# Performance work log

Hardware: AMD Instinct MI355X
Metric: run time of the kernel (lower is better)

Reference implementation:

```python
import jax, jax.numpy as jnp
import numpy as np

N, K, H, E_IN = 4096, 48, 128, 384
SCALE = 30.0
EPS = 1e-5


def _gelu(x):
    return jax.nn.gelu(x, approximate=False)


def _ln(x, s, o):
    m = jnp.mean(x, axis=-1, keepdims=True)
    v = jnp.var(x, axis=-1, keepdims=True)
    return (x - m) * jax.lax.rsqrt(v + EPS) * s + o


def setup_inputs() -> dict:
    key = jax.random.key(0)
    ks = jax.random.split(key, 12)
    init = lambda k, shp: (jax.random.normal(k, shp, jnp.float32) * 0.02)
    return {
        "h_V": jax.random.normal(ks[0], (N, H), jnp.float32),
        "h_E": jax.random.normal(ks[1], (N, K, E_IN), jnp.float32),
        "mask_V": jnp.ones((N,), jnp.float32),
        "mask_attend": jnp.ones((N, K), jnp.float32),
        "W1_w": init(ks[2], (H + E_IN, H)), "W1_b": jnp.zeros((H,), jnp.float32),
        "W2_w": init(ks[3], (H, H)), "W2_b": jnp.zeros((H,), jnp.float32),
        "W3_w": init(ks[4], (H, H)), "W3_b": jnp.zeros((H,), jnp.float32),
        "Win_w": init(ks[5], (H, 4 * H)), "Win_b": jnp.zeros((4 * H,), jnp.float32),
        "Wout_w": init(ks[6], (4 * H, H)), "Wout_b": jnp.zeros((H,), jnp.float32),
        "norm1_s": jnp.ones((H,), jnp.float32), "norm1_o": jnp.zeros((H,), jnp.float32),
        "norm2_s": jnp.ones((H,), jnp.float32), "norm2_o": jnp.zeros((H,), jnp.float32),
    }


def reference(h_V, h_E, mask_V, mask_attend,
              W1_w, W1_b, W2_w, W2_b, W3_w, W3_b,
              Win_w, Win_b, Wout_w, Wout_b,
              norm1_s, norm1_o, norm2_s, norm2_o):
    # expand node features over K neighbors and concat with edge features: [N,K,H+E_IN]
    h_V_expand = jnp.broadcast_to(h_V[:, None, :], (h_V.shape[0], h_E.shape[1], h_V.shape[1]))
    h_EV = jnp.concatenate([h_V_expand, h_E], axis=-1)
    # 3-layer GELU MLP on each edge token
    h = _gelu(jnp.einsum('nke,eh->nkh', h_EV, W1_w) + W1_b)
    h = _gelu(jnp.einsum('nkh,hg->nkg', h, W2_w) + W2_b)
    h_message = jnp.einsum('nkg,gh->nkh', h, W3_w) + W3_b
    # masked sum-reduce over neighbors
    h_message = mask_attend[..., None] * h_message
    dh = jnp.sum(h_message, axis=-2) / SCALE
    h_Vn = _ln(h_V + dh, norm1_s, norm1_o)  # dropout rate = 0.0 -> identity
    # position-wise FFN
    dh = _gelu(h_Vn @ Win_w + Win_b) @ Wout_w + Wout_b
    h_Vn = _ln(h_Vn + dh, norm2_s, norm2_o)
    return mask_V[:, None] * h_Vn
```

## Files before the change

kernel.cpp:

```cpp
#include <hip/hip_runtime.h>
#include <hip/hip_bf16.h>
#include <math.h>

typedef __attribute__((ext_vector_type(8))) __bf16 bf16x8;
typedef __attribute__((ext_vector_type(4))) float f32x4;

#define OFF_W1P    0
#define OFF_W2P    65536
#define OFF_W3P    81920
#define OFF_WINP   98304
#define OFF_WOUTP  163840
#define NPACK      229376
#define OFF_DH_BYTES 458752

__device__ __forceinline__ float gelu_f(float x) {
  float t = 1.5957691216f * x * (1.0f + 0.044715f * x * x);
  return __fdividef(x, 1.0f + __expf(-t));
}

__device__ __forceinline__ bf16x8 cvt8(float4 u, float4 v) {
  bf16x8 r;
  r[0] = (__bf16)u.x; r[1] = (__bf16)u.y; r[2] = (__bf16)u.z; r[3] = (__bf16)u.w;
  r[4] = (__bf16)v.x; r[5] = (__bf16)v.y; r[6] = (__bf16)v.z; r[7] = (__bf16)v.w;
  return r;
}

__device__ __forceinline__ void gload_lds16(const void* g, void* l) {
  __builtin_amdgcn_global_load_lds(
      (const __attribute__((address_space(1))) void*)g,
      (__attribute__((address_space(3))) void*)l, 16, 0, 0);
}

#define MFMA __builtin_amdgcn_mfma_f32_16x16x32_bf16

__global__ __launch_bounds__(256) void prep_kernel(
    const float* __restrict__ W1, const float* __restrict__ W2,
    const float* __restrict__ W3, const float* __restrict__ Wi,
    const float* __restrict__ Wo, __bf16* __restrict__ wsb)
{
  int i = blockIdx.x * 256 + threadIdx.x;
  float v;
  if (i < 65536) {
    int j = i;
    int jj = j & 7, ln = (j >> 3) & 63, n = (j >> 9) & 7, ks = j >> 12;
    int k = ks * 32 + (ln >> 4) * 8 + jj, h = n * 16 + (ln & 15);
    v = W1[k * 128 + h];
  } else if (i < 81920) {
    int j = i - 65536;
    int jj = j & 7, ln = (j >> 3) & 63, n = (j >> 9) & 7, ks = j >> 12;
    int k = ks * 32 + (ln >> 4) * 8 + jj, g = n * 16 + (ln & 15);
    v = W2[k * 128 + g];
  } else if (i < 98304) {
    int j = i - 81920;
    int jj = j & 7, ln = (j >> 3) & 63, n = (j >> 9) & 7, ks = j >> 12;
    int k = ks * 32 + (ln >> 4) * 8 + jj, h = n * 16 + (ln & 15);
    v = W3[k * 128 + h];
  } else if (i < 163840) {
    int j = i - 98304;
    int jj = j & 7, ln = (j >> 3) & 63, n = (j >> 9) & 31, ks = j >> 14;
    int k = ks * 32 + (ln >> 4) * 8 + jj, o = n * 16 + (ln & 15);
    v = Wi[k * 512 + o];
  } else {
    int j = i - 163840;
    int jj = j & 7, ln = (j >> 3) & 63, n = (j >> 9) & 7, ks = j >> 12;
    int k = ks * 32 + (ln >> 4) * 8 + jj, h = n * 16 + (ln & 15);
    v = Wo[k * 128 + h];
  }
  wsb[i] = (__bf16)v;
}

__global__ __launch_bounds__(256, 4) void edge_mlp_kernel(
    const float* __restrict__ hE, const float* __restrict__ hV,
    const float* __restrict__ mask_att, const __bf16* __restrict__ wsb,
    const float* __restrict__ b1, const float* __restrict__ b2,
    const float* __restrict__ b3, float* __restrict__ dh)
{
  __shared__ char lds[24576];

  const int tid = threadIdx.x;
  const int w = tid >> 6, lane = tid & 63;
  const int lo = lane & 15, hi = lane >> 4;
  const int n0 = blockIdx.x * 2;

  const __bf16* W1p = wsb + OFF_W1P;

  f32x4 acc[2][3][2];
#pragma unroll
  for (int nl = 0; nl < 2; nl++)
#pragma unroll
    for (int m = 0; m < 3; m++)
#pragma unroll
      for (int nn = 0; nn < 2; nn++) {
        acc[nl][m][nn][0] = 0.f; acc[nl][m][nn][1] = 0.f;
        acc[nl][m][nn][2] = 0.f; acc[nl][m][nn][3] = 0.f;
      }

  const char* gsrc[3];
  int ldst[3];
#pragma unroll
  for (int j = 0; j < 3; j++) {
    int o = w * 3072 + j * 1024 + lane * 16;
    int r = o >> 7;
    int p = (o >> 4) & 7;
    int lcol = p ^ (r & 7);
    int nl = (r >= 48) ? 1 : 0, kk = r - nl * 48;
    gsrc[j] = (const char*)(hE + (size_t)((n0 + nl) * 48 + kk) * 384 + lcol * 4);
    ldst[j] = w * 3072 + j * 1024;
  }

#pragma unroll
  for (int j = 0; j < 3; j++) gload_lds16(gsrc[j],       &lds[ldst[j]]);
#pragma unroll
  for (int j = 0; j < 3; j++) gload_lds16(gsrc[j] + 128, &lds[12288 + ldst[j]]);

#pragma unroll 1
  for (int ks = 0; ks < 4; ++ks) {
    const float* v0 = hV + (n0)     * 128 + ks * 32 + hi * 8;
    const float* v1 = hV + (n0 + 1) * 128 + ks * 32 + hi * 8;
    bf16x8 a0 = cvt8(*(const float4*)v0, *(const float4*)(v0 + 4));
    bf16x8 a1 = cvt8(*(const float4*)v1, *(const float4*)(v1 + 4));
#pragma unroll
    for (int nn = 0; nn < 2; nn++) {
      bf16x8 b = *(const bf16x8*)(W1p + ((ks * 8 + w * 2 + nn) << 9) + lane * 8);
#pragma unroll
      for (int m = 0; m < 3; m++) {
        acc[0][m][nn] = MFMA(a0, b, acc[0][m][nn], 0, 0, 0);
        acc[1][m][nn] = MFMA(a1, b, acc[1][m][nn], 0, 0, 0);
      }
    }
  }

  bf16x8 bbc[2], bbn[2];
#pragma unroll
  for (int nn = 0; nn < 2; nn++)
    bbc[nn] = *(const bf16x8*)(W1p + ((4 * 8 + w * 2 + nn) << 9) + lane * 8);

  const int swz0 = (2 * hi) ^ (lo & 7);
  const int swz1 = (2 * hi + 1) ^ (lo & 7);

#pragma unroll 1
  for (int i = 0; i < 12; ++i) {
    if (i < 11) asm volatile("s_waitcnt vmcnt(3)\n\ts_barrier" ::: "memory");
    else        asm volatile("s_waitcnt vmcnt(0)\n\ts_barrier" ::: "memory");

    if (i < 11) {
#pragma unroll
      for (int nn = 0; nn < 2; nn++)
        bbn[nn] = *(const bf16x8*)(W1p + (((5 + i) * 8 + w * 2 + nn) << 9) + lane * 8);
    }

    const char* Ab = lds + (i & 1) * 12288;
    bf16x8 a[2][3];
#pragma unroll
    for (int nl = 0; nl < 2; nl++)
#pragma unroll
      for (int m = 0; m < 3; m++) {
        int r = nl * 48 + m * 16 + lo;
        const char* rb = Ab + r * 128;
        float4 u = *(const float4*)(rb + swz0 * 16);
        float4 v = *(const float4*)(rb + swz1 * 16);
        a[nl][m] = cvt8(u, v);
      }
#pragma unroll
    for (int nn = 0; nn < 2; nn++)
#pragma unroll
      for (int nl = 0; nl < 2; nl++)
#pragma unroll
        for (int m = 0; m < 3; m++)
          acc[nl][m][nn] = MFMA(a[nl][m], bbc[nn], acc[nl][m][nn], 0, 0, 0);

    asm volatile("s_waitcnt lgkmcnt(0)\n\ts_barrier" ::: "memory");
    if (i < 10) {
      const int of = (i + 2) * 128;
#pragma unroll
      for (int j = 0; j < 3; j++)
        gload_lds16(gsrc[j] + of, &lds[(i & 1) * 12288 + ldst[j]]);
    }
    if (i < 11) { bbc[0] = bbn[0]; bbc[1] = bbn[1]; }
  }

#pragma unroll 1
  for (int layer = 0; layer < 2; ++layer) {
    const float*  bv = layer ? b2 : b1;
    const __bf16* Wp = wsb + (layer ? OFF_W3P : OFF_W2P);
    __syncthreads();
#pragma unroll
    for (int nn = 0; nn < 2; nn++) {
      int col = (w * 2 + nn) * 16 + lo;
      float bc = bv[col];
#pragma unroll
      for (int nl = 0; nl < 2; nl++)
#pragma unroll
        for (int m = 0; m < 3; m++)
#pragma unroll
          for (int i = 0; i < 4; i++) {
            int row = nl * 48 + m * 16 + hi * 4 + i;
            float g = gelu_f(acc[nl][m][nn][i] + bc);
            *(__bf16*)(lds + row * 256 + ((col * 2) ^ ((row & 7) << 4))) = (__bf16)g;
            acc[nl][m][nn][i] = 0.f;
          }
    }
    __syncthreads();
#pragma unroll 1
    for (int kc2 = 0; kc2 < 2; ++kc2) {
#pragma unroll
      for (int ks32 = 0; ks32 < 2; ++ks32) {
        int ks = kc2 * 2 + ks32;
        bf16x8 bb[2];
#pragma unroll
        for (int nn = 0; nn < 2; nn++)
          bb[nn] = *(const bf16x8*)(Wp + ((ks * 8 + w * 2 + nn) << 9) + lane * 8);
        bf16x8 a[2][3];
#pragma unroll
        for (int nl = 0; nl < 2; nl++)
#pragma unroll
          for (int m = 0; m < 3; m++) {
            int row = nl * 48 + m * 16 + lo;
            a[nl][m] = *(const bf16x8*)(lds + row * 256 + ((kc2 * 128 + ks32 * 64 + hi * 16) ^ ((row & 7) << 4)));
          }
#pragma unroll
        for (int nn = 0; nn < 2; nn++)
#pragma unroll
          for (int nl = 0; nl < 2; nl++)
#pragma unroll
            for (int m = 0; m < 3; m++)
              acc[nl][m][nn] = MFMA(a[nl][m], bb[nn], acc[nl][m][nn], 0, 0, 0);
      }
    }
  }

#pragma unroll
  for (int nl = 0; nl < 2; nl++) {
    float msk[12];
#pragma unroll
    for (int m = 0; m < 3; m++)
#pragma unroll
      for (int i = 0; i < 4; i++)
        msk[m * 4 + i] = mask_att[(n0 + nl) * 48 + m * 16 + hi * 4 + i];
#pragma unroll
    for (int nn = 0; nn < 2; nn++) {
      int col = (w * 2 + nn) * 16 + lo;
      float bc = b3[col];
      float s = 0.f;
#pragma unroll
      for (int m = 0; m < 3; m++)
#pragma unroll
        for (int i = 0; i < 4; i++)
          s += (acc[nl][m][nn][i] + bc) * msk[m * 4 + i];
      s += __shfl_xor(s, 16);
      s += __shfl_xor(s, 32);
      if (hi == 0)
        dh[(n0 + nl) * 128 + col] = s * (1.0f / 30.0f);
    }
  }
}

__global__ __launch_bounds__(256, 2) void node_ffn_kernel(
    const float* __restrict__ hV, const float* __restrict__ maskV,
    const __bf16* __restrict__ wsb, const float* __restrict__ dh,
    const float* __restrict__ Winb, const float* __restrict__ Woutb,
    const float* __restrict__ ns1, const float* __restrict__ no1,
    const float* __restrict__ ns2, const float* __restrict__ no2,
    float* __restrict__ out)
{
  __shared__ char lds2[36864];
  char*  xA  = lds2;
  float* hvn = (float*)(lds2 + 4096);
  char*  A2  = lds2 + 12288;
  float* red = (float*)(lds2 + 28672);

  const __bf16* Winp  = wsb + OFF_WINP;
  const __bf16* Woutp = wsb + OFF_WOUTP;

  const int tid = threadIdx.x;
  const int w = tid >> 6, lane = tid & 63;
  const int lo = lane & 15, hi = lane >> 4;
  const int n0 = blockIdx.x * 16;

  const int row = tid >> 4;
  const int sg  = tid & 15;
  const int node = n0 + row;

  {
    const float* pv = hV + node * 128 + sg * 8;
    const float* pd = dh + node * 128 + sg * 8;
    float4 a0 = *(const float4*)pv;
    float4 a1 = *(const float4*)(pv + 4);
    float4 d0 = *(const float4*)pd;
    float4 d1 = *(const float4*)(pd + 4);
    float x[8] = { a0.x + d0.x, a0.y + d0.y, a0.z + d0.z, a0.w + d0.w,
                   a1.x + d1.x, a1.y + d1.y, a1.z + d1.z, a1.w + d1.w };
    float s = 0.f, sq = 0.f;
#pragma unroll
    for (int j = 0; j < 8; j++) { s += x[j]; sq += x[j] * x[j]; }
#pragma unroll
    for (int off = 8; off >= 1; off >>= 1) { s += __shfl_xor(s, off); sq += __shfl_xor(sq, off); }
    float mean = s * (1.f / 128.f);
    float var  = sq * (1.f / 128.f) - mean * mean;
    float rs = rsqrtf(var + 1e-5f);
    bf16x8 vb;
    float yv[8];
#pragma unroll
    for (int j = 0; j < 8; j++) {
      int col = sg * 8 + j;
      float y = (x[j] - mean) * rs * ns1[col] + no1[col];
      yv[j] = y; vb[j] = (__bf16)y;
    }
    *(float4*)(hvn + row * 128 + sg * 8)     = make_float4(yv[0], yv[1], yv[2], yv[3]);
    *(float4*)(hvn + row * 128 + sg * 8 + 4) = make_float4(yv[4], yv[5], yv[6], yv[7]);
    *(bf16x8*)(xA + row * 256 + ((sg * 16) ^ ((row & 7) << 4))) = vb;
  }
  __syncthreads();

  f32x4 acc[8];
#pragma unroll
  for (int n = 0; n < 8; n++) { acc[n][0] = 0.f; acc[n][1] = 0.f; acc[n][2] = 0.f; acc[n][3] = 0.f; }
#pragma unroll
  for (int ks = 0; ks < 4; ks++) {
    const int kb = (ks * 32 + hi * 8) * 2;
    bf16x8 a = *(const bf16x8*)(xA + lo * 256 + (kb ^ ((lo & 7) << 4)));
#pragma unroll
    for (int n = 0; n < 8; n++) {
      int ng = w * 8 + n;
      bf16x8 b = *(const bf16x8*)(Winp + ((ks * 32 + ng) << 9) + lane * 8);
      acc[n] = MFMA(a, b, acc[n], 0, 0, 0);
    }
  }
#pragma unroll
  for (int n = 0; n < 8; n++) {
    int col = w * 128 + n * 16 + lo;
    float bc = Winb[col];
#pragma unroll
    for (int i = 0; i < 4; i++) {
      int r2 = hi * 4 + i;
      float g = gelu_f(acc[n][i] + bc);
      *(__bf16*)(A2 + r2 * 1024 + ((col * 2) ^ ((r2 & 7) << 4))) = (__bf16)g;
    }
  }
  __syncthreads();

  f32x4 acc2[2];
  acc2[0][0] = 0.f; acc2[0][1] = 0.f; acc2[0][2] = 0.f; acc2[0][3] = 0.f;
  acc2[1][0] = 0.f; acc2[1][1] = 0.f; acc2[1][2] = 0.f; acc2[1][3] = 0.f;
#pragma unroll
  for (int ks = 0; ks < 16; ks++) {
    const int kb = (ks * 32 + hi * 8) * 2;
    bf16x8 a = *(const bf16x8*)(A2 + lo * 1024 + (kb ^ ((lo & 7) << 4)));
#pragma unroll
    for (int n = 0; n < 2; n++) {
      int ng = w * 2 + n;
      bf16x8 b = *(const bf16x8*)(Woutp + ((ks * 8 + ng) << 9) + lane * 8);
      acc2[n] = MFMA(a, b, acc2[n], 0, 0, 0);
    }
  }
#pragma unroll
  for (int n = 0; n < 2; n++) {
    int col = w * 32 + n * 16 + lo;
    float bc = Woutb[col];
#pragma unroll
    for (int i = 0; i < 4; i++) {
      int r2 = hi * 4 + i;
      red[r2 * 128 + col] = acc2[n][i] + bc;
    }
  }
  __syncthreads();

  {
    const float* ph = hvn + row * 128 + sg * 8;
    const float* pr = red + row * 128 + sg * 8;
    float4 h0 = *(const float4*)ph;
    float4 h1 = *(const float4*)(ph + 4);
    float4 r0 = *(const float4*)pr;
    float4 r1 = *(const float4*)(pr + 4);
    float x[8] = { h0.x + r0.x, h0.y + r0.y, h0.z + r0.z, h0.w + r0.w,
                   h1.x + r1.x, h1.y + r1.y, h1.z + r1.z, h1.w + r1.w };
    float s = 0.f, sq = 0.f;
#pragma unroll
    for (int j = 0; j < 8; j++) { s += x[j]; sq += x[j] * x[j]; }
#pragma unroll
    for (int off = 8; off >= 1; off >>= 1) { s += __shfl_xor(s, off); sq += __shfl_xor(sq, off); }
    float mean = s * (1.f / 128.f);
    float var  = sq * (1.f / 128.f) - mean * mean;
    float rs = rsqrtf(var + 1e-5f);
    float mv = maskV[node];
    float o[8];
#pragma unroll
    for (int j = 0; j < 8; j++) {
      int col = sg * 8 + j;
      o[j] = mv * ((x[j] - mean) * rs * ns2[col] + no2[col]);
    }
    *(float4*)(out + node * 128 + sg * 8)     = make_float4(o[0], o[1], o[2], o[3]);
    *(float4*)(out + node * 128 + sg * 8 + 4) = make_float4(o[4], o[5], o[6], o[7]);
  }
}

extern "C" void kernel_launch(void* const* d_in, const int* in_sizes, int n_in,
                              void* d_out, int out_size, void* d_ws, size_t ws_size,
                              hipStream_t stream)
{
  (void)in_sizes; (void)n_in; (void)out_size; (void)ws_size;
  const float* hV   = (const float*)d_in[0];
  const float* hE   = (const float*)d_in[1];
  const float* mV   = (const float*)d_in[2];
  const float* mAtt = (const float*)d_in[3];
  const float* W1   = (const float*)d_in[4];
  const float* b1   = (const float*)d_in[5];
  const float* W2   = (const float*)d_in[6];
  const float* b2   = (const float*)d_in[7];
  const float* W3   = (const float*)d_in[8];
  const float* b3   = (const float*)d_in[9];
  const float* Win  = (const float*)d_in[10];
  const float* binb = (const float*)d_in[11];
  const float* Wout = (const float*)d_in[12];
  const float* bout = (const float*)d_in[13];
  const float* ns1  = (const float*)d_in[14];
  const float* no1  = (const float*)d_in[15];
  const float* ns2  = (const float*)d_in[16];
  const float* no2  = (const float*)d_in[17];

  __bf16* wsb = (__bf16*)d_ws;
  float* dh   = (float*)((char*)d_ws + OFF_DH_BYTES);
  float* out  = (float*)d_out;

  prep_kernel<<<NPACK / 256, 256, 0, stream>>>(W1, W2, W3, Win, Wout, wsb);
  edge_mlp_kernel<<<2048, 256, 0, stream>>>(hE, hV, mAtt, wsb, b1, b2, b3, dh);
  node_ffn_kernel<<<256, 256, 0, stream>>>(hV, mV, wsb, dh, binb, bout,
                                           ns1, no1, ns2, no2, out);
}
```

Before: 111.8 us.

## Triple-buffer edge-feature LDS staging and deepen W1 prefetch in edge MLP

Switches the h_E chunk streaming in the edge MLP from double to triple buffering in LDS. W1 B-fragments are now prefetched two chunks ahead, and the chunk loop is fully unrolled with adjusted vmcnt waits. This hides more global-load latency, but LDS grows to 36KB and launch bounds drop from 4 to 3 blocks per SIMD, which lowers occupancy and raises register pressure.

```diff
diff --git a/kernel.cpp b/kernel.cpp
--- a/kernel.cpp
+++ b/kernel.cpp
@@ -69,13 +69,13 @@
   wsb[i] = (__bf16)v;
 }
 
-__global__ __launch_bounds__(256, 4) void edge_mlp_kernel(
+__global__ __launch_bounds__(256, 3) void edge_mlp_kernel(
     const float* __restrict__ hE, const float* __restrict__ hV,
     const float* __restrict__ mask_att, const __bf16* __restrict__ wsb,
     const float* __restrict__ b1, const float* __restrict__ b2,
     const float* __restrict__ b3, float* __restrict__ dh)
 {
-  __shared__ char lds[24576];
+  __shared__ char lds[36864];
 
   const int tid = threadIdx.x;
   const int w = tid >> 6, lane = tid & 63;
@@ -108,10 +108,16 @@
     ldst[j] = w * 3072 + j * 1024;
   }
 
-#pragma unroll
-  for (int j = 0; j < 3; j++) gload_lds16(gsrc[j],       &lds[ldst[j]]);
-#pragma unroll
-  for (int j = 0; j < 3; j++) gload_lds16(gsrc[j] + 128, &lds[12288 + ldst[j]]);
+  bf16x8 bbs[3][2];
+
+#define STAGE(ch, buf) \
+  { _Pragma("unroll") for (int j = 0; j < 3; j++) \
+      gload_lds16(gsrc[j] + (ch) * 128, &lds[(buf) * 12288 + ldst[j]]); }
+#define BBLOAD(ch, set) \
+  { _Pragma("unroll") for (int nn = 0; nn < 2; nn++) \
+      bbs[set][nn] = *(const bf16x8*)(W1p + ((((ch) + 4) * 8 + w * 2 + nn) << 9) + lane * 8); }
+
+  STAGE(0, 0); BBLOAD(0, 0); STAGE(1, 1); BBLOAD(1, 1); STAGE(2, 2);
 
 #pragma unroll 1
   for (int ks = 0; ks < 4; ++ks) {
@@ -130,53 +136,40 @@
     }
   }
 
-  bf16x8 bbc[2], bbn[2];
-#pragma unroll
-  for (int nn = 0; nn < 2; nn++)
-    bbc[nn] = *(const bf16x8*)(W1p + ((4 * 8 + w * 2 + nn) << 9) + lane * 8);
-
   const int swz0 = (2 * hi) ^ (lo & 7);
   const int swz1 = (2 * hi + 1) ^ (lo & 7);
 
-#pragma unroll 1
+#pragma unroll
   for (int i = 0; i < 12; ++i) {
-    if (i < 11) asm volatile("s_waitcnt vmcnt(3)\n\ts_barrier" ::: "memory");
-    else        asm volatile("s_waitcnt vmcnt(0)\n\ts_barrier" ::: "memory");
-
-    if (i < 11) {
+    if (i <= 9)       asm volatile("s_waitcnt vmcnt(8)\n\ts_barrier" ::: "memory");
+    else if (i == 10) asm volatile("s_waitcnt vmcnt(5)\n\ts_barrier" ::: "memory");
+    else              asm volatile("s_waitcnt vmcnt(0)\n\ts_barrier" ::: "memory");
+
+    {
+      const char* Ab = lds + (i % 3) * 12288;
+      bf16x8 a[2][3];
+#pragma unroll
+      for (int nl = 0; nl < 2; nl++)
+#pragma unroll
+        for (int m = 0; m < 3; m++) {
+          int r = nl * 48 + m * 16 + lo;
+          const char* rb = Ab + r * 128;
+          float4 u = *(const float4*)(rb + swz0 * 16);
+          float4 v = *(const float4*)(rb + swz1 * 16);
+          a[nl][m] = cvt8(u, v);
+        }
 #pragma unroll
       for (int nn = 0; nn < 2; nn++)
-        bbn[nn] = *(const bf16x8*)(W1p + (((5 + i) * 8 + w * 2 + nn) << 9) + lane * 8);
-    }
-
-    const char* Ab = lds + (i & 1) * 12288;
-    bf16x8 a[2][3];
-#pragma unroll
-    for (int nl = 0; nl < 2; nl++)
-#pragma unroll
-      for (int m = 0; m < 3; m++) {
-        int r = nl * 48 + m * 16 + lo;
-        const char* rb = Ab + r * 128;
-        float4 u = *(const float4*)(rb + swz0 * 16);
-        float4 v = *(const float4*)(rb + swz1 * 16);
-        a[nl][m] = cvt8(u, v);
-      }
-#pragma unroll
-    for (int nn = 0; nn < 2; nn++)
-#pragma unroll
-      for (int nl = 0; nl < 2; nl++)
-#pragma unroll
-        for (int m = 0; m < 3; m++)
-          acc[nl][m][nn] = MFMA(a[nl][m], bbc[nn], acc[nl][m][nn], 0, 0, 0);
+#pragma unroll
+        for (int nl = 0; nl < 2; nl++)
+#pragma unroll
+          for (int m = 0; m < 3; m++)
+            acc[nl][m][nn] = MFMA(a[nl][m], bbs[i % 3][nn], acc[nl][m][nn], 0, 0, 0);
+    }
 
     asm volatile("s_waitcnt lgkmcnt(0)\n\ts_barrier" ::: "memory");
-    if (i < 10) {
-      const int of = (i + 2) * 128;
-#pragma unroll
-      for (int j = 0; j < 3; j++)
-        gload_lds16(gsrc[j] + of, &lds[(i & 1) * 12288 + ldst[j]]);
-    }
-    if (i < 11) { bbc[0] = bbn[0]; bbc[1] = bbn[1]; }
+    if (i + 2 <= 11) BBLOAD(i + 2, (i + 2) % 3);
+    if (i + 3 <= 11) STAGE(i + 3, i % 3);
   }
 
 #pragma unroll 1
@@ -253,6 +246,8 @@
         dh[(n0 + nl) * 128 + col] = s * (1.0f / 30.0f);
     }
   }
+#undef STAGE
+#undef BBLOAD
 }
 
 __global__ __launch_bounds__(256, 2) void node_ffn_kernel(
```

Result: slower. 115.7 us (+3.5%).
